# Kernel tuning notes

Measured on AMD Instinct MI355X. Metric: run time of the kernel, lower is better.

The kernel has to match this reference:

```python
import jax, jax.numpy as jnp
import numpy as np

N_T, N_S, F_IN, H, N_OUT = 2048, 512, 7, 64, 3


def setup_inputs() -> dict:
    key = jax.random.key(0)
    ks = jax.random.split(key, 12)
    pts = jax.random.normal(ks[0], (N_T, 3), jnp.float32)
    centers = jax.random.normal(ks[1], (N_S, 3), jnp.float32)
    nrm = jax.random.normal(ks[2], (N_S, 3), jnp.float32)
    normals = nrm / jnp.linalg.norm(nrm, axis=-1, keepdims=True)
    areas = jax.random.uniform(ks[3], (N_S,), jnp.float32, 0.1, 1.0)
    ref_lengths = jax.random.uniform(ks[4], (2,), jnp.float32, 0.5, 1.5)

    def lin(k, i, o):
        return jax.random.normal(k, (i, o), jnp.float32) / np.float32(np.sqrt(i))

    return {
        "prediction_points": pts,
        "face_centers": centers,
        "face_normals": normals,
        "face_areas": areas,
        "reference_lengths": ref_lengths,
        "W1": lin(ks[5], F_IN, H), "b1": jnp.zeros((H,), jnp.float32),
        "W2": lin(ks[6], H, H),    "b2": jnp.zeros((H,), jnp.float32),
        "W3": lin(ks[7], H, H),    "b3": jnp.zeros((H,), jnp.float32),
        "Wout": lin(ks[8], H, N_OUT), "bout": jnp.zeros((N_OUT,), jnp.float32),
        "p_scale": jnp.float32(1.0), "p_bias": jnp.float32(0.0),
        "v_scale": jnp.float32(1.0), "v_bias": jnp.float32(0.0),
    }


def reference(prediction_points, face_centers, face_normals, face_areas,
              reference_lengths, W1, b1, W2, b2, W3, b3, Wout, bout,
              p_scale, p_bias, v_scale, v_bias):
    eps = jnp.float32(1e-8)
    # Pairwise relative geometry (translation/rotation-equivariant features).
    rvec = prediction_points[:, None, :] - face_centers[None, :, :]  # [T,S,3]
    r2 = jnp.sum(rvec * rvec, axis=-1)                               # [T,S]
    r = jnp.sqrt(r2 + eps)
    rhat = rvec / r[..., None]
    c = jnp.sum(rhat * face_normals[None, :, :], axis=-1)            # cos(angle)
    # Legendre polynomials P0..P3 (n_spherical_harmonics = 4).
    legendre = jnp.stack(
        [jnp.ones_like(c), c, 0.5 * (3.0 * c * c - 1.0),
         0.5 * (5.0 * c * c * c - 3.0 * c)], axis=-1)                # [T,S,4]
    # Multiscale nondimensional distance features, one per reference length.
    dfeat = 1.0 / (1.0 + r[..., None] / reference_lengths)           # [T,S,2]
    afeat = jnp.broadcast_to(jnp.log(face_areas)[None, :, None],
                             r.shape + (1,))                          # [T,S,1]
    feats = jnp.concatenate([dfeat, legendre, afeat], axis=-1)       # [T,S,7]
    # Kernel MLP evaluated per (target, source) pair.
    h = jnp.tanh(feats @ W1 + b1)
    h = jnp.tanh(h @ W2 + b2)
    h = jnp.tanh(h @ W3 + b3)
    out = h @ Wout + bout                                            # [T,S,3]
    # Green's-function-like decay, area-weighted boundary integral.
    decay = face_areas[None, :] / (r2 + 1.0)                         # [T,S]
    p = jnp.sum(out[..., 0] * decay, axis=1)                         # [T]
    vel = jnp.sum((out[..., 1:2] * rhat
                   + out[..., 2:3] * face_normals[None, :, :])
                  * decay[..., None], axis=1)                        # [T,3]
    pressure = p * p_scale + p_bias
    velocity = vel * v_scale + v_bias
    return jnp.concatenate([pressure[:, None], velocity], axis=-1)   # [T,4]
```

## Files before the change

### kernel.cpp

```cpp
#include <hip/hip_runtime.h>
#include <hip/hip_fp16.h>


#define N_T 2048
#define N_S 512
#define BLK 128
#define WPB 2
#define SCALE 2.885390081777927f

typedef _Float16 f16;
typedef _Float16 f16x8 __attribute__((ext_vector_type(8)));
typedef _Float16 f16x4 __attribute__((ext_vector_type(4)));
typedef float f32x4 __attribute__((ext_vector_type(4)));
typedef unsigned short u16;

__device__ __forceinline__ float tanh_s(float x) {
    float e = __builtin_amdgcn_exp2f(x);
    return fmaf(-2.0f, __builtin_amdgcn_rcpf(e + 1.0f), 1.0f);
}

__device__ __forceinline__ f32x4 mfma16h(f16x8 a, f16x8 b, f32x4 c) {
    return __builtin_amdgcn_mfma_f32_16x16x32_f16(a, b, c, 0, 0, 0);
}

#define DENSE_LAYER(WARR, BPTR)                                                \
    {                                                                          \
        _Pragma("unroll")                                                      \
        for (int n4 = 0; n4 < 4; ++n4) {                                       \
            const int row = n4 * 16 + l15;                                     \
            const f16x8 bfa = *(const f16x8*)&hb[row][q * 8];                  \
            const f16x8 bfb = *(const f16x8*)&hb[row][32 + q * 8];             \
            f32x4 c[4];                                                        \
            _Pragma("unroll")                                                  \
            for (int mt = 0; mt < 4; ++mt) {                                   \
                const float4 b = BPTR[mt * 4 + q];                             \
                c[mt] = (f32x4){b.x * SCALE, b.y * SCALE,                      \
                                b.z * SCALE, b.w * SCALE};                     \
            }                                                                  \
            _Pragma("unroll")                                                  \
            for (int mt = 0; mt < 4; ++mt)                                     \
                c[mt] = mfma16h(WARR[mt], bfa, c[mt]);                         \
            _Pragma("unroll")                                                  \
            for (int mt = 0; mt < 4; ++mt)                                     \
                c[mt] = mfma16h(WARR[4 + mt], bfb, c[mt]);                     \
            _Pragma("unroll")                                                  \
            for (int mt = 0; mt < 4; ++mt) {                                   \
                f16x4 o;                                                       \
                o[0] = (f16)tanh_s(c[mt][0]);                                  \
                o[1] = (f16)tanh_s(c[mt][1]);                                  \
                o[2] = (f16)tanh_s(c[mt][2]);                                  \
                o[3] = (f16)tanh_s(c[mt][3]);                                  \
                *(f16x4*)&hb[row][mt * 16 + q * 4] = o;                        \
            }                                                                  \
        }                                                                      \
    }

__global__ __launch_bounds__(BLK, 2) void globe_mfma(
    const float* __restrict__ pts, const float* __restrict__ ctr,
    const float* __restrict__ nrm, const float* __restrict__ areas,
    const float* __restrict__ rlen,
    const float* __restrict__ W1, const float* __restrict__ b1,
    const float* __restrict__ W2, const float* __restrict__ b2,
    const float* __restrict__ W3, const float* __restrict__ b3,
    const float* __restrict__ Wout, const float* __restrict__ bout,
    const float* __restrict__ p_scale, const float* __restrict__ p_bias,
    const float* __restrict__ v_scale, const float* __restrict__ v_bias,
    float* __restrict__ out)
{
    __shared__ __align__(16) u16 hbuf[WPB][64][72];
    __shared__ __align__(16) float geom[WPB][64][8];

    const int tid  = threadIdx.x;
    const int lane = tid & 63;
    const int wv   = tid >> 6;
    const int l15  = lane & 15;
    const int q    = lane >> 4;
    const int t    = blockIdx.x * WPB + wv;

    f16x8 w1h[4], w1l[4];
    f16x8 w2f[8], w3f[8];
    f16x8 woh[2], wol[2];
    #pragma unroll
    for (int mt = 0; mt < 4; ++mt) {
        f16x8 vh, vl;
        #pragma unroll
        for (int j = 0; j < 8; ++j) {
            const float x = (q == 0 && j < 7) ? W1[j * 64 + mt * 16 + l15] * SCALE : 0.f;
            const f16 h = (f16)x;
            vh[j] = h;
            vl[j] = (f16)(x - (float)h);
        }
        w1h[mt] = vh; w1l[mt] = vl;
    }
    #pragma unroll
    for (int ks = 0; ks < 2; ++ks)
        #pragma unroll
        for (int mt = 0; mt < 4; ++mt) {
            f16x8 v;
            #pragma unroll
            for (int j = 0; j < 8; ++j)
                v[j] = (f16)(W2[(ks * 32 + q * 8 + j) * 64 + mt * 16 + l15] * SCALE);
            w2f[ks * 4 + mt] = v;
        }
    #pragma unroll
    for (int ks = 0; ks < 2; ++ks)
        #pragma unroll
        for (int mt = 0; mt < 4; ++mt) {
            f16x8 v;
            #pragma unroll
            for (int j = 0; j < 8; ++j)
                v[j] = (f16)(W3[(ks * 32 + q * 8 + j) * 64 + mt * 16 + l15] * SCALE);
            w3f[ks * 4 + mt] = v;
        }
    #pragma unroll
    for (int ks = 0; ks < 2; ++ks) {
        f16x8 vh, vl;
        #pragma unroll
        for (int j = 0; j < 8; ++j) {
            const float x = (l15 < 3) ? Wout[(ks * 32 + q * 8 + j) * 3 + l15] : 0.f;
            const f16 h = (f16)x;
            vh[j] = h;
            vl[j] = (f16)(x - (float)h);
        }
        woh[ks] = vh; wol[ks] = vl;
    }

    const float px = pts[3 * t + 0], py = pts[3 * t + 1], pz = pts[3 * t + 2];
    const float invL0 = __builtin_amdgcn_rcpf(rlen[0]);
    const float invL1 = __builtin_amdgcn_rcpf(rlen[1]);
    f32x4 co_init = (f32x4){0.f, 0.f, 0.f, 0.f};
    if (q == 0) { co_init[0] = bout[0]; co_init[1] = bout[1]; co_init[2] = bout[2]; }

    const float4* __restrict__ b1v4 = (const float4*)b1;
    const float4* __restrict__ b2v4 = (const float4*)b2;
    const float4* __restrict__ b3v4 = (const float4*)b3;

    u16 (*hb)[72] = hbuf[wv];
    float (*gm)[8] = geom[wv];
    const f16x8 fzero = (f16x8){0, 0, 0, 0, 0, 0, 0, 0};

    float accp = 0.f, avx = 0.f, avy = 0.f, avz = 0.f;

    #pragma unroll 1
    for (int ch = 0; ch < 8; ++ch) {
        const int s = ch * 64 + lane;
        const float cx = ctr[3 * s + 0], cy = ctr[3 * s + 1], cz = ctr[3 * s + 2];
        const float snx = nrm[3 * s + 0], sny = nrm[3 * s + 1], snz = nrm[3 * s + 2];
        const float ar = areas[s];
        const float rvx = px - cx, rvy = py - cy, rvz = pz - cz;
        const float r2 = rvx * rvx + rvy * rvy + rvz * rvz;
        const float r2e = r2 + 1e-8f;
        const float rinv = __builtin_amdgcn_rsqf(r2e);
        const float r = r2e * rinv;
        const float rhx = rvx * rinv, rhy = rvy * rinv, rhz = rvz * rinv;
        const float cth = rhx * snx + rhy * sny + rhz * snz;
        const float c2 = cth * cth;
        const float decay = ar * __builtin_amdgcn_rcpf(r2 + 1.0f);
        {
            f16x8 fv;
            fv[0] = (f16)(__builtin_amdgcn_rcpf(fmaf(r, invL0, 1.0f)));
            fv[1] = (f16)(__builtin_amdgcn_rcpf(fmaf(r, invL1, 1.0f)));
            fv[2] = (f16)1.0f;
            fv[3] = (f16)cth;
            fv[4] = (f16)fmaf(1.5f, c2, -0.5f);
            fv[5] = (f16)(cth * fmaf(2.5f, c2, -1.5f));
            fv[6] = (f16)__logf(ar);
            fv[7] = (f16)0.0f;
            *(f16x8*)&hb[lane][0] = fv;
        }
        *(float4*)&gm[lane][0] = make_float4(decay, rhx, rhy, rhz);
        *(float4*)&gm[lane][4] = make_float4(snx, sny, snz, 0.f);

        #pragma unroll
        for (int n4 = 0; n4 < 4; ++n4) {
            const int row = n4 * 16 + l15;
            const f16x8 lv = *(const f16x8*)&hb[row][0];
            const f16x8 bf = (q == 0) ? lv : fzero;
            f32x4 c[4];
            #pragma unroll
            for (int mt = 0; mt < 4; ++mt) {
                const float4 b = b1v4[mt * 4 + q];
                c[mt] = (f32x4){b.x * SCALE, b.y * SCALE, b.z * SCALE, b.w * SCALE};
            }
            #pragma unroll
            for (int mt = 0; mt < 4; ++mt) c[mt] = mfma16h(w1h[mt], bf, c[mt]);
            #pragma unroll
            for (int mt = 0; mt < 4; ++mt) c[mt] = mfma16h(w1l[mt], bf, c[mt]);
            #pragma unroll
            for (int mt = 0; mt < 4; ++mt) {
                f16x4 o;
                o[0] = (f16)tanh_s(c[mt][0]);
                o[1] = (f16)tanh_s(c[mt][1]);
                o[2] = (f16)tanh_s(c[mt][2]);
                o[3] = (f16)tanh_s(c[mt][3]);
                *(f16x4*)&hb[row][mt * 16 + q * 4] = o;
            }
        }

        DENSE_LAYER(w2f, b2v4)
        DENSE_LAYER(w3f, b3v4)

        #pragma unroll
        for (int n4 = 0; n4 < 4; ++n4) {
            const int row = n4 * 16 + l15;
            const f16x8 bfa = *(const f16x8*)&hb[row][q * 8];
            const f16x8 bfb = *(const f16x8*)&hb[row][32 + q * 8];
            f32x4 co = co_init;
            co = mfma16h(woh[0], bfa, co);
            co = mfma16h(wol[0], bfa, co);
            co = mfma16h(woh[1], bfb, co);
            co = mfma16h(wol[1], bfb, co);
            if (q == 0) {
                const float4 g1 = *(const float4*)&gm[row][0];
                const float4 g2 = *(const float4*)&gm[row][4];
                const float o0 = co[0], o1 = co[1], o2 = co[2];
                accp = fmaf(o0, g1.x, accp);
                avx  = fmaf(fmaf(o1, g1.y, o2 * g2.x), g1.x, avx);
                avy  = fmaf(fmaf(o1, g1.z, o2 * g2.y), g1.x, avy);
                avz  = fmaf(fmaf(o1, g1.w, o2 * g2.z), g1.x, avz);
            }
        }
    }

    #pragma unroll
    for (int off = 8; off > 0; off >>= 1) {
        accp += __shfl_down(accp, off);
        avx  += __shfl_down(avx,  off);
        avy  += __shfl_down(avy,  off);
        avz  += __shfl_down(avz,  off);
    }

    if (lane == 0) {
        const float ps = p_scale[0], pb = p_bias[0];
        const float vs = v_scale[0], vb = v_bias[0];
        out[4 * t + 0] = fmaf(accp, ps, pb);
        out[4 * t + 1] = fmaf(avx, vs, vb);
        out[4 * t + 2] = fmaf(avy, vs, vb);
        out[4 * t + 3] = fmaf(avz, vs, vb);
    }
}

extern "C" void kernel_launch(void* const* d_in, const int* in_sizes, int n_in,
                              void* d_out, int out_size, void* d_ws, size_t ws_size,
                              hipStream_t stream) {
    (void)in_sizes; (void)n_in; (void)d_ws; (void)ws_size; (void)out_size;
    const float* pts   = (const float*)d_in[0];
    const float* ctr   = (const float*)d_in[1];
    const float* nrm   = (const float*)d_in[2];
    const float* areas = (const float*)d_in[3];
    const float* rlen  = (const float*)d_in[4];
    const float* W1    = (const float*)d_in[5];
    const float* b1    = (const float*)d_in[6];
    const float* W2    = (const float*)d_in[7];
    const float* b2    = (const float*)d_in[8];
    const float* W3    = (const float*)d_in[9];
    const float* b3    = (const float*)d_in[10];
    const float* Wout  = (const float*)d_in[11];
    const float* bout  = (const float*)d_in[12];
    const float* ps    = (const float*)d_in[13];
    const float* pb    = (const float*)d_in[14];
    const float* vs    = (const float*)d_in[15];
    const float* vb    = (const float*)d_in[16];

    globe_mfma<<<N_T / WPB, BLK, 0, stream>>>(
        pts, ctr, nrm, areas, rlen, W1, b1, W2, b2, W3, b3, Wout, bout,
        ps, pb, vs, vb, (float*)d_out);
}
```

Measured before the change: 149.4 us.

## Prepack MLP weights in a prep kernel and split sources across two blocks

Adds a small prep kernel that converts the MLP weights to packed fp16 MFMA fragments, stores the pre-scaled biases in the workspace, and zeroes the output. The main kernel now loads the prepacked fragments instead of converting weights in every block. Each target is split across two single-wave blocks that each handle half the sources and combine their partial sums with atomicAdd. The geometry stored in LDS is packed to fp16 to cut LDS footprint. This trades an extra launch, atomics and reduced geometry precision for more parallelism and less per-block setup.

```diff
diff --git a/kernel.cpp b/kernel.cpp
--- a/kernel.cpp
+++ b/kernel.cpp
@@ -4,8 +4,6 @@
 
 #define N_T 2048
 #define N_S 512
-#define BLK 128
-#define WPB 2
 #define SCALE 2.885390081777927f
 
 typedef _Float16 f16;
@@ -13,6 +11,7 @@
 typedef _Float16 f16x4 __attribute__((ext_vector_type(4)));
 typedef float f32x4 __attribute__((ext_vector_type(4)));
 typedef unsigned short u16;
+typedef unsigned int u32;
 
 __device__ __forceinline__ float tanh_s(float x) {
     float e = __builtin_amdgcn_exp2f(x);
@@ -23,19 +22,76 @@
     return __builtin_amdgcn_mfma_f32_16x16x32_f16(a, b, c, 0, 0, 0);
 }
 
-#define DENSE_LAYER(WARR, BPTR)                                                \
+__global__ __launch_bounds__(256) void prep_kernel(
+    const float* __restrict__ W1, const float* __restrict__ b1,
+    const float* __restrict__ W2, const float* __restrict__ b2,
+    const float* __restrict__ W3, const float* __restrict__ b3,
+    const float* __restrict__ Wout,
+    float* __restrict__ ws, float* __restrict__ out)
+{
+    const int tid = blockIdx.x * 256 + threadIdx.x;
+    ((float4*)out)[tid] = make_float4(0.f, 0.f, 0.f, 0.f);
+
+    const int fid = tid >> 6, lane = tid & 63;
+    const int q = lane >> 4, l15 = lane & 15;
+
+    if (fid < 28) {
+        float x[8];
+        bool lo = false;
+        if (fid < 8) {
+            const int mt = fid & 3;
+            lo = (fid >= 4);
+            #pragma unroll
+            for (int j = 0; j < 8; ++j)
+                x[j] = (q == 0 && j < 7) ? W1[j * 64 + mt * 16 + l15] * SCALE : 0.f;
+        } else if (fid < 16) {
+            const int k = fid - 8, ks = k >> 2, mt = k & 3;
+            #pragma unroll
+            for (int j = 0; j < 8; ++j)
+                x[j] = W2[(ks * 32 + q * 8 + j) * 64 + mt * 16 + l15] * SCALE;
+        } else if (fid < 24) {
+            const int k = fid - 16, ks = k >> 2, mt = k & 3;
+            #pragma unroll
+            for (int j = 0; j < 8; ++j)
+                x[j] = W3[(ks * 32 + q * 8 + j) * 64 + mt * 16 + l15] * SCALE;
+        } else {
+            const int ks = fid & 1;
+            lo = (fid >= 26);
+            #pragma unroll
+            for (int j = 0; j < 8; ++j)
+                x[j] = (l15 < 3) ? Wout[(ks * 32 + q * 8 + j) * 3 + l15] : 0.f;
+        }
+        f16x8 v;
+        #pragma unroll
+        for (int j = 0; j < 8; ++j) {
+            const f16 h = (f16)x[j];
+            v[j] = lo ? (f16)(x[j] - (float)h) : h;
+        }
+        *(f16x8*)((char*)ws + ((fid * 64 + lane) << 4)) = v;
+    }
+
+    if (tid >= 1792 && tid < 1984) {
+        const int Lb = (tid - 1792) >> 6, i = tid & 63;
+        float bv;
+        if (Lb == 0)      bv = b1[i];
+        else if (Lb == 1) bv = b2[i];
+        else              bv = b3[i];
+        ws[7168 + (Lb * 64 + i)] = bv * SCALE;
+    }
+}
+
+#define DENSE_LAYER(WARR, LIDX)                                                \
     {                                                                          \
         _Pragma("unroll")                                                      \
         for (int n4 = 0; n4 < 4; ++n4) {                                       \
             const int row = n4 * 16 + l15;                                     \
-            const f16x8 bfa = *(const f16x8*)&hb[row][q * 8];                  \
-            const f16x8 bfb = *(const f16x8*)&hb[row][32 + q * 8];             \
+            const f16x8 bfa = *(const f16x8*)&hbuf[row][q * 8];                \
+            const f16x8 bfb = *(const f16x8*)&hbuf[row][32 + q * 8];           \
             f32x4 c[4];                                                        \
             _Pragma("unroll")                                                  \
             for (int mt = 0; mt < 4; ++mt) {                                   \
-                const float4 b = BPTR[mt * 4 + q];                             \
-                c[mt] = (f32x4){b.x * SCALE, b.y * SCALE,                      \
-                                b.z * SCALE, b.w * SCALE};                     \
+                const float4 b = wsB[(LIDX) * 16 + mt * 4 + q];                \
+                c[mt] = (f32x4){b.x, b.y, b.z, b.w};                           \
             }                                                                  \
             _Pragma("unroll")                                                  \
             for (int mt = 0; mt < 4; ++mt)                                     \
@@ -50,80 +106,45 @@
                 o[1] = (f16)tanh_s(c[mt][1]);                                  \
                 o[2] = (f16)tanh_s(c[mt][2]);                                  \
                 o[3] = (f16)tanh_s(c[mt][3]);                                  \
-                *(f16x4*)&hb[row][mt * 16 + q * 4] = o;                        \
+                *(f16x4*)&hbuf[row][mt * 16 + q * 4] = o;                      \
             }                                                                  \
         }                                                                      \
     }
 
-__global__ __launch_bounds__(BLK, 2) void globe_mfma(
+__global__ __launch_bounds__(64, 4) void globe_mfma(
     const float* __restrict__ pts, const float* __restrict__ ctr,
     const float* __restrict__ nrm, const float* __restrict__ areas,
-    const float* __restrict__ rlen,
-    const float* __restrict__ W1, const float* __restrict__ b1,
-    const float* __restrict__ W2, const float* __restrict__ b2,
-    const float* __restrict__ W3, const float* __restrict__ b3,
-    const float* __restrict__ Wout, const float* __restrict__ bout,
+    const float* __restrict__ rlen, const float* __restrict__ bout,
     const float* __restrict__ p_scale, const float* __restrict__ p_bias,
     const float* __restrict__ v_scale, const float* __restrict__ v_bias,
+    const float* __restrict__ ws,
     float* __restrict__ out)
 {
-    __shared__ __align__(16) u16 hbuf[WPB][64][72];
-    __shared__ __align__(16) float geom[WPB][64][8];
-
-    const int tid  = threadIdx.x;
-    const int lane = tid & 63;
-    const int wv   = tid >> 6;
+    __shared__ __align__(16) u16 hbuf[64][72];
+    __shared__ __align__(16) uint4 geomP[64];
+
+    const int lane = threadIdx.x;
     const int l15  = lane & 15;
     const int q    = lane >> 4;
-    const int t    = blockIdx.x * WPB + wv;
-
-    f16x8 w1h[4], w1l[4];
-    f16x8 w2f[8], w3f[8];
-    f16x8 woh[2], wol[2];
-    #pragma unroll
-    for (int mt = 0; mt < 4; ++mt) {
-        f16x8 vh, vl;
-        #pragma unroll
-        for (int j = 0; j < 8; ++j) {
-            const float x = (q == 0 && j < 7) ? W1[j * 64 + mt * 16 + l15] * SCALE : 0.f;
-            const f16 h = (f16)x;
-            vh[j] = h;
-            vl[j] = (f16)(x - (float)h);
-        }
-        w1h[mt] = vh; w1l[mt] = vl;
-    }
-    #pragma unroll
-    for (int ks = 0; ks < 2; ++ks)
-        #pragma unroll
-        for (int mt = 0; mt < 4; ++mt) {
-            f16x8 v;
-            #pragma unroll
-            for (int j = 0; j < 8; ++j)
-                v[j] = (f16)(W2[(ks * 32 + q * 8 + j) * 64 + mt * 16 + l15] * SCALE);
-            w2f[ks * 4 + mt] = v;
-        }
-    #pragma unroll
-    for (int ks = 0; ks < 2; ++ks)
-        #pragma unroll
-        for (int mt = 0; mt < 4; ++mt) {
-            f16x8 v;
-            #pragma unroll
-            for (int j = 0; j < 8; ++j)
-                v[j] = (f16)(W3[(ks * 32 + q * 8 + j) * 64 + mt * 16 + l15] * SCALE);
-            w3f[ks * 4 + mt] = v;
-        }
-    #pragma unroll
-    for (int ks = 0; ks < 2; ++ks) {
-        f16x8 vh, vl;
-        #pragma unroll
-        for (int j = 0; j < 8; ++j) {
-            const float x = (l15 < 3) ? Wout[(ks * 32 + q * 8 + j) * 3 + l15] : 0.f;
-            const f16 h = (f16)x;
-            vh[j] = h;
-            vl[j] = (f16)(x - (float)h);
-        }
-        woh[ks] = vh; wol[ks] = vl;
-    }
+    const int t    = blockIdx.x >> 1;
+    const int hf   = blockIdx.x & 1;
+
+    const f16x8* __restrict__ wsF = (const f16x8*)ws;
+    const float4* __restrict__ wsB = (const float4*)(ws + 7168);
+
+    f16x8 w1h[4], w1l[4], w2f[8], w3f[8], woh[2], wol[2];
+    #pragma unroll
+    for (int mt = 0; mt < 4; ++mt) w1h[mt] = wsF[(0 + mt) * 64 + lane];
+    #pragma unroll
+    for (int mt = 0; mt < 4; ++mt) w1l[mt] = wsF[(4 + mt) * 64 + lane];
+    #pragma unroll
+    for (int k = 0; k < 8; ++k)    w2f[k]  = wsF[(8 + k) * 64 + lane];
+    #pragma unroll
+    for (int k = 0; k < 8; ++k)    w3f[k]  = wsF[(16 + k) * 64 + lane];
+    #pragma unroll
+    for (int k = 0; k < 2; ++k)    woh[k]  = wsF[(24 + k) * 64 + lane];
+    #pragma unroll
+    for (int k = 0; k < 2; ++k)    wol[k]  = wsF[(26 + k) * 64 + lane];
 
     const float px = pts[3 * t + 0], py = pts[3 * t + 1], pz = pts[3 * t + 2];
     const float invL0 = __builtin_amdgcn_rcpf(rlen[0]);
@@ -131,19 +152,12 @@
     f32x4 co_init = (f32x4){0.f, 0.f, 0.f, 0.f};
     if (q == 0) { co_init[0] = bout[0]; co_init[1] = bout[1]; co_init[2] = bout[2]; }
 
-    const float4* __restrict__ b1v4 = (const float4*)b1;
-    const float4* __restrict__ b2v4 = (const float4*)b2;
-    const float4* __restrict__ b3v4 = (const float4*)b3;
-
-    u16 (*hb)[72] = hbuf[wv];
-    float (*gm)[8] = geom[wv];
     const f16x8 fzero = (f16x8){0, 0, 0, 0, 0, 0, 0, 0};
-
     float accp = 0.f, avx = 0.f, avy = 0.f, avz = 0.f;
 
     #pragma unroll 1
-    for (int ch = 0; ch < 8; ++ch) {
-        const int s = ch * 64 + lane;
+    for (int i = 0; i < 4; ++i) {
+        const int s = (hf * 4 + i) * 64 + lane;
         const float cx = ctr[3 * s + 0], cy = ctr[3 * s + 1], cz = ctr[3 * s + 2];
         const float snx = nrm[3 * s + 0], sny = nrm[3 * s + 1], snz = nrm[3 * s + 2];
         const float ar = areas[s];
@@ -166,21 +180,27 @@
             fv[5] = (f16)(cth * fmaf(2.5f, c2, -1.5f));
             fv[6] = (f16)__logf(ar);
             fv[7] = (f16)0.0f;
-            *(f16x8*)&hb[lane][0] = fv;
-        }
-        *(float4*)&gm[lane][0] = make_float4(decay, rhx, rhy, rhz);
-        *(float4*)&gm[lane][4] = make_float4(snx, sny, snz, 0.f);
+            *(f16x8*)&hbuf[lane][0] = fv;
+        }
+        {
+            uint4 g;
+            g.x = __builtin_bit_cast(u32, decay);
+            g.y = __builtin_bit_cast(u32, __floats2half2_rn(rhx, rhy));
+            g.z = __builtin_bit_cast(u32, __floats2half2_rn(rhz, snx));
+            g.w = __builtin_bit_cast(u32, __floats2half2_rn(sny, snz));
+            geomP[lane] = g;
+        }
 
         #pragma unroll
         for (int n4 = 0; n4 < 4; ++n4) {
             const int row = n4 * 16 + l15;
-            const f16x8 lv = *(const f16x8*)&hb[row][0];
+            const f16x8 lv = *(const f16x8*)&hbuf[row][0];
             const f16x8 bf = (q == 0) ? lv : fzero;
             f32x4 c[4];
             #pragma unroll
             for (int mt = 0; mt < 4; ++mt) {
-                const float4 b = b1v4[mt * 4 + q];
-                c[mt] = (f32x4){b.x * SCALE, b.y * SCALE, b.z * SCALE, b.w * SCALE};
+                const float4 b = wsB[mt * 4 + q];
+                c[mt] = (f32x4){b.x, b.y, b.z, b.w};
             }
             #pragma unroll
             for (int mt = 0; mt < 4; ++mt) c[mt] = mfma16h(w1h[mt], bf, c[mt]);
@@ -193,31 +213,34 @@
                 o[1] = (f16)tanh_s(c[mt][1]);
                 o[2] = (f16)tanh_s(c[mt][2]);
                 o[3] = (f16)tanh_s(c[mt][3]);
-                *(f16x4*)&hb[row][mt * 16 + q * 4] = o;
+                *(f16x4*)&hbuf[row][mt * 16 + q * 4] = o;
             }
         }
 
-        DENSE_LAYER(w2f, b2v4)
-        DENSE_LAYER(w3f, b3v4)
+        DENSE_LAYER(w2f, 1)
+        DENSE_LAYER(w3f, 2)
 
         #pragma unroll
         for (int n4 = 0; n4 < 4; ++n4) {
             const int row = n4 * 16 + l15;
-            const f16x8 bfa = *(const f16x8*)&hb[row][q * 8];
-            const f16x8 bfb = *(const f16x8*)&hb[row][32 + q * 8];
+            const f16x8 bfa = *(const f16x8*)&hbuf[row][q * 8];
+            const f16x8 bfb = *(const f16x8*)&hbuf[row][32 + q * 8];
             f32x4 co = co_init;
             co = mfma16h(woh[0], bfa, co);
             co = mfma16h(wol[0], bfa, co);
             co = mfma16h(woh[1], bfb, co);
             co = mfma16h(wol[1], bfb, co);
             if (q == 0) {
-                const float4 g1 = *(const float4*)&gm[row][0];
-                const float4 g2 = *(const float4*)&gm[row][4];
+                const uint4 g = geomP[row];
+                const float d = __builtin_bit_cast(float, g.x);
+                const float2 rxy = __half22float2(__builtin_bit_cast(__half2, g.y));
+                const float2 rzx = __half22float2(__builtin_bit_cast(__half2, g.z));
+                const float2 nyz = __half22float2(__builtin_bit_cast(__half2, g.w));
                 const float o0 = co[0], o1 = co[1], o2 = co[2];
-                accp = fmaf(o0, g1.x, accp);
-                avx  = fmaf(fmaf(o1, g1.y, o2 * g2.x), g1.x, avx);
-                avy  = fmaf(fmaf(o1, g1.z, o2 * g2.y), g1.x, avy);
-                avz  = fmaf(fmaf(o1, g1.w, o2 * g2.z), g1.x, avz);
+                accp = fmaf(o0, d, accp);
+                avx  = fmaf(fmaf(o1, rxy.x, o2 * rzx.y), d, avx);
+                avy  = fmaf(fmaf(o1, rxy.y, o2 * nyz.x), d, avy);
+                avz  = fmaf(fmaf(o1, rzx.x, o2 * nyz.y), d, avz);
             }
         }
     }
@@ -233,17 +256,17 @@
     if (lane == 0) {
         const float ps = p_scale[0], pb = p_bias[0];
         const float vs = v_scale[0], vb = v_bias[0];
-        out[4 * t + 0] = fmaf(accp, ps, pb);
-        out[4 * t + 1] = fmaf(avx, vs, vb);
-        out[4 * t + 2] = fmaf(avy, vs, vb);
-        out[4 * t + 3] = fmaf(avz, vs, vb);
+        atomicAdd(&out[4 * t + 0], fmaf(accp, ps, 0.5f * pb));
+        atomicAdd(&out[4 * t + 1], fmaf(avx, vs, 0.5f * vb));
+        atomicAdd(&out[4 * t + 2], fmaf(avy, vs, 0.5f * vb));
+        atomicAdd(&out[4 * t + 3], fmaf(avz, vs, 0.5f * vb));
     }
 }
 
 extern "C" void kernel_launch(void* const* d_in, const int* in_sizes, int n_in,
                               void* d_out, int out_size, void* d_ws, size_t ws_size,
                               hipStream_t stream) {
-    (void)in_sizes; (void)n_in; (void)d_ws; (void)ws_size; (void)out_size;
+    (void)in_sizes; (void)n_in; (void)ws_size; (void)out_size;
     const float* pts   = (const float*)d_in[0];
     const float* ctr   = (const float*)d_in[1];
     const float* nrm   = (const float*)d_in[2];
@@ -261,8 +284,10 @@
     const float* pb    = (const float*)d_in[14];
     const float* vs    = (const float*)d_in[15];
     const float* vb    = (const float*)d_in[16];
-
-    globe_mfma<<<N_T / WPB, BLK, 0, stream>>>(
-        pts, ctr, nrm, areas, rlen, W1, b1, W2, b2, W3, b3, Wout, bout,
-        ps, pb, vs, vb, (float*)d_out);
-}
+    float* ws = (float*)d_ws;
+
+    prep_kernel<<<8, 256, 0, stream>>>(W1, b1, W2, b2, W3, b3, Wout,
+                                       ws, (float*)d_out);
+    globe_mfma<<<2 * N_T, 64, 0, stream>>>(
+        pts, ctr, nrm, areas, rlen, bout, ps, pb, vs, vb, ws, (float*)d_out);
+}
```

Result: slower. 182.0 us (+21.8%).
